# Performance work log

Hardware: AMD Instinct MI355X
Metric: run time of the kernel (lower is better)

The kernel has to match this reference:

```python
import jax, jax.numpy as jnp
import numpy as np

HIDDEN = 1024
N_HEADS = 16
HEAD_DIM = HIDDEN // N_HEADS
WINDOW = 256
HALF_W = WINDOW // 2  # 128
GLOBAL_TOKENS = (0,)


def setup_inputs() -> dict:
    key = jax.random.key(0)
    ks = jax.random.split(key, 5)
    B, S = 1, 4096
    scale = 0.02
    return {
        "x": jax.random.normal(ks[0], (B, S, HIDDEN), dtype=jnp.float32),
        "Wq": jax.random.normal(ks[1], (HIDDEN, HIDDEN), dtype=jnp.float32) * scale,
        "Wk": jax.random.normal(ks[2], (HIDDEN, HIDDEN), dtype=jnp.float32) * scale,
        "Wv": jax.random.normal(ks[3], (HIDDEN, HIDDEN), dtype=jnp.float32) * scale,
        "Wo": jax.random.normal(ks[4], (HIDDEN, HIDDEN), dtype=jnp.float32) * scale,
    }


def _longformer_mask(seq_len: int) -> jnp.ndarray:
    # sliding window |i-j| <= half_w, plus full rows/cols for global tokens
    idx = jnp.arange(seq_len)
    mask = jnp.abs(idx[:, None] - idx[None, :]) <= HALF_W
    for g in GLOBAL_TOKENS:
        if 0 <= g < seq_len:
            mask = mask.at[g, :].set(True)
            mask = mask.at[:, g].set(True)
    return mask  # [S, S] bool


def reference(x, Wq, Wk, Wv, Wo):
    B, S, H = x.shape
    scale = HEAD_DIM ** -0.5
    # nn.Linear(bias=False): y = x @ W.T ; split heads -> [B, nH, S, hd]
    def proj(W):
        return jnp.einsum('bsh,oh->bso', x, W).reshape(B, S, N_HEADS, HEAD_DIM).transpose(0, 2, 1, 3)
    q, k, v = proj(Wq), proj(Wk), proj(Wv)
    scores = jnp.einsum('bnsd,bntd->bnst', q, k) * scale  # [B, nH, S, S]
    mask = _longformer_mask(S)
    scores = jnp.where(mask[None, None], scores, jnp.float32(-jnp.inf))
    attn = jax.nn.softmax(scores, axis=-1)
    out = jnp.einsum('bnst,bntd->bnsd', attn, v)  # [B, nH, S, hd]
    out = out.transpose(0, 2, 1, 3).reshape(B, S, H)
    return jnp.einsum('bsh,oh->bso', out, Wo)
```

## Files before the change

### kernel.cpp

```cpp
#include <hip/hip_runtime.h>
#include <hip/hip_bf16.h>
#include <stdint.h>

#define S_LEN 4096
#define HID   1024
#define NH    16
#define HD    64
#define HWIN  128

typedef __bf16 bf16x8 __attribute__((ext_vector_type(8)));
typedef float  f32x4  __attribute__((ext_vector_type(4)));
typedef unsigned short u16x8 __attribute__((ext_vector_type(8)));

typedef const __attribute__((address_space(1))) unsigned int* gas_ptr;
typedef __attribute__((address_space(3))) unsigned int* las_ptr;

__device__ __forceinline__ float bf2f(unsigned short u) {
  union { float f; uint32_t i; } w; w.i = ((uint32_t)u) << 16; return w.f;
}
__device__ __forceinline__ unsigned short f2bf(float f) {
  union { float f; uint32_t i; } w; w.f = f;
  uint32_t r = (w.i + 0x7FFFu + ((w.i >> 16) & 1u)) >> 16;
  return (unsigned short)r;
}

__device__ __forceinline__ void gld_lds16(const void* g, void* l) {
  __builtin_amdgcn_global_load_lds((gas_ptr)g, (las_ptr)l, 16, 0, 0);
}

__global__ __launch_bounds__(256) void convert_all(
    const float* __restrict__ x,
    const float* __restrict__ wq, const float* __restrict__ wk,
    const float* __restrict__ wv, const float* __restrict__ wo,
    unsigned short* __restrict__ xb,
    unsigned short* __restrict__ wqb, unsigned short* __restrict__ wkb,
    unsigned short* __restrict__ wvb, unsigned short* __restrict__ wob) {
  const float* in; unsigned short* out; int n4;
  switch (blockIdx.y) {
    case 0:  in = x;  out = xb;  n4 = (S_LEN * HID) / 4; break;
    case 1:  in = wq; out = wqb; n4 = (HID * HID) / 4;   break;
    case 2:  in = wk; out = wkb; n4 = (HID * HID) / 4;   break;
    case 3:  in = wv; out = wvb; n4 = (HID * HID) / 4;   break;
    default: in = wo; out = wob; n4 = (HID * HID) / 4;   break;
  }
  int i = blockIdx.x * 256 + threadIdx.x;
  if (i >= n4) return;
  float4 v = reinterpret_cast<const float4*>(in)[i];
  ushort4 o;
  o.x = f2bf(v.x); o.y = f2bf(v.y); o.z = f2bf(v.z); o.w = f2bf(v.w);
  reinterpret_cast<ushort4*>(out)[i] = o;
}

__device__ __forceinline__ void gemm_body(const unsigned short* __restrict__ A,
                                          const unsigned short* __restrict__ B,
                                          unsigned short* __restrict__ Cb,
                                          float* __restrict__ Cf, int mode) {
  __shared__ __align__(16) unsigned short As[128 * 64];
  __shared__ __align__(16) unsigned short Bs[128 * 64];
  constexpr int K = HID;
  const int tid  = threadIdx.x;
  const int lane = tid & 63;
  const int wave = tid >> 6;
  const int wm = wave >> 1, wn = wave & 1;
  const int m0 = blockIdx.x * 128;
  const int n0 = blockIdx.y * 128;
  const int cl = lane & 15, g = lane >> 4;

  f32x4 acc[4][4];
#pragma unroll
  for (int i = 0; i < 4; i++)
#pragma unroll
    for (int j = 0; j < 4; j++) acc[i][j] = f32x4{0.f, 0.f, 0.f, 0.f};

  const unsigned short* Ap[4];
  const unsigned short* Bp[4];
  int ldso[4];
#pragma unroll
  for (int u = 0; u < 4; u++) {
    int s = tid + u * 256;
    int row = s >> 3, c16 = s & 7;
    int sc = ((c16 ^ (row & 7)) << 3);
    Ap[u] = A + (size_t)(m0 + row) * K + sc;
    Bp[u] = B + (size_t)(n0 + row) * K + sc;
    ldso[u] = s * 8;
  }

  for (int k0 = 0; k0 < K; k0 += 64) {
#pragma unroll
    for (int u = 0; u < 4; u++) {
      gld_lds16(Ap[u] + k0, &As[ldso[u]]);
      gld_lds16(Bp[u] + k0, &Bs[ldso[u]]);
    }
    __syncthreads();
#pragma unroll
    for (int kk = 0; kk < 2; kk++) {
      bf16x8 a[4], b[4];
#pragma unroll
      for (int mi = 0; mi < 4; mi++) {
        int row = wm * 64 + mi * 16 + cl;
        int c16 = (kk * 4 + g) ^ (row & 7);
        a[mi] = *reinterpret_cast<const bf16x8*>(&As[row * 64 + c16 * 8]);
      }
#pragma unroll
      for (int ni = 0; ni < 4; ni++) {
        int row = wn * 64 + ni * 16 + cl;
        int c16 = (kk * 4 + g) ^ (row & 7);
        b[ni] = *reinterpret_cast<const bf16x8*>(&Bs[row * 64 + c16 * 8]);
      }
#pragma unroll
      for (int mi = 0; mi < 4; mi++)
#pragma unroll
        for (int ni = 0; ni < 4; ni++)
          acc[mi][ni] = __builtin_amdgcn_mfma_f32_16x16x32_bf16(a[mi], b[ni], acc[mi][ni], 0, 0, 0);
    }
    __syncthreads();
  }

  const int rl = g * 4;
#pragma unroll
  for (int mi = 0; mi < 4; mi++)
#pragma unroll
    for (int ni = 0; ni < 4; ni++)
#pragma unroll
      for (int i = 0; i < 4; i++) {
        int r = m0 + wm * 64 + mi * 16 + rl + i;
        int c = n0 + wn * 64 + ni * 16 + cl;
        float v = acc[mi][ni][i];
        if (mode == 2)      Cf[(size_t)r * HID + c] = v;
        else if (mode == 1) Cb[(size_t)c * S_LEN + r] = f2bf(v);
        else                Cb[(size_t)r * HID + c] = f2bf(v);
      }
}

__global__ __launch_bounds__(256, 2) void gemm_qkv(
    const unsigned short* __restrict__ xb,
    const unsigned short* __restrict__ wqb, const unsigned short* __restrict__ wkb,
    const unsigned short* __restrict__ wvb,
    unsigned short* __restrict__ Qb, unsigned short* __restrict__ Kb,
    unsigned short* __restrict__ Vt) {
  const unsigned short* B = (blockIdx.z == 0) ? wqb : (blockIdx.z == 1) ? wkb : wvb;
  unsigned short* C       = (blockIdx.z == 0) ? Qb  : (blockIdx.z == 1) ? Kb  : Vt;
  int mode = (blockIdx.z == 2) ? 1 : 0;
  gemm_body(xb, B, C, nullptr, mode);
}

__global__ __launch_bounds__(256, 2) void gemm_proj(
    const unsigned short* __restrict__ Ob, const unsigned short* __restrict__ wob,
    float* __restrict__ out) {
  gemm_body(Ob, wob, nullptr, out, 2);
}

__global__ __launch_bounds__(256) void attn_win(
    const unsigned short* __restrict__ Qb,
    const unsigned short* __restrict__ Kb,
    const unsigned short* __restrict__ Vt,
    unsigned short* __restrict__ Ob,
    float* __restrict__ mw, float* __restrict__ lw, float* __restrict__ ow) {
  const int tid  = threadIdx.x;
  const int lane = tid & 63;
  const int wave = tid >> 6;

  if (blockIdx.x >= 1024) {
    const int bid = blockIdx.x - 1024;
    const int c = bid & 15, h = bid >> 4;
    const int k = c * 256 + tid;
    __shared__ float qsh[HD];
    __shared__ float ps[256];
    __shared__ float redm[4], redl[4];
    __shared__ float red2[4][HD];
    const float LOG2E = 1.44269504f;

    if (tid < HD) qsh[tid] = bf2f(Qb[h * HD + tid]);
    __syncthreads();

    const unsigned short* kr = Kb + (size_t)k * HID + h * HD;
    float acc = 0.f;
#pragma unroll
    for (int v8 = 0; v8 < 8; v8++) {
      u16x8 kv = *reinterpret_cast<const u16x8*>(kr + v8 * 8);
#pragma unroll
      for (int j = 0; j < 8; j++) acc += qsh[v8 * 8 + j] * bf2f(kv[j]);
    }
    float s = acc * 0.125f;

    float m = s;
#pragma unroll
    for (int d = 1; d < 64; d <<= 1) m = fmaxf(m, __shfl_xor(m, d, 64));
    if (lane == 0) redm[wave] = m;
    __syncthreads();
    float m_c = fmaxf(fmaxf(redm[0], redm[1]), fmaxf(redm[2], redm[3]));

    float p = exp2f((s - m_c) * LOG2E);
    ps[tid] = p;
    float l = p;
#pragma unroll
    for (int d = 1; d < 64; d <<= 1) l += __shfl_xor(l, d, 64);
    if (lane == 0) redl[wave] = l;
    __syncthreads();
    float l_c = redl[0] + redl[1] + redl[2] + redl[3];

    const int d = tid & 63, grp = tid >> 6;
    const unsigned short* vrow = Vt + (size_t)(h * HD + d) * S_LEN + c * 256 + grp * 64;
    float a2 = 0.f;
#pragma unroll
    for (int v8 = 0; v8 < 8; v8++) {
      u16x8 vv = *reinterpret_cast<const u16x8*>(vrow + v8 * 8);
#pragma unroll
      for (int j = 0; j < 8; j++) a2 += ps[grp * 64 + v8 * 8 + j] * bf2f(vv[j]);
    }
    red2[grp][d] = a2;
    __syncthreads();
    if (tid < HD) {
      float o = red2[0][tid] + red2[1][tid] + red2[2][tid] + red2[3][tid];
      ow[(size_t)(h * 16 + c) * HD + tid] = o;
    }
    if (tid == 0) { mw[h * 16 + c] = m_c; lw[h * 16 + c] = l_c; }
    return;
  }

  __shared__ __align__(16) unsigned short Kl[2][64 * 64];
  __shared__ __align__(16) unsigned short Vl[2][64 * 64];
  __shared__ __align__(16) unsigned short Ps[4][16 * 64];
  const int L  = (blockIdx.x & 7) * 128 + (blockIdx.x >> 3);
  const int h  = L >> 6;
  const int q0 = (L & 63) * 64;
  const int qr   = q0 + wave * 16;
  const int cl = lane & 15, g = lane >> 4, rl = g * 4;
  const float SCL = 0.125f * 1.44269504f;

  int kw0 = q0 - 128; if (kw0 < 0) kw0 = 0;
  int kw1 = q0 + 192; if (kw1 > S_LEN) kw1 = S_LEN;
  const int nc = (kw1 - kw0) >> 6;

  const int s0 = tid, s1 = tid + 256;
  const int kr0 = s0 >> 3, kc0 = ((s0 & 7) ^ (kr0 & 7)) << 3;
  const int kr1 = s1 >> 3, kc1 = ((s1 & 7) ^ (kr1 & 7)) << 3;
  const unsigned short* Kbase = Kb + h * HD;
  const unsigned short* Vbase = Vt + (size_t)h * HD * S_LEN;

  auto stage = [&](int kb, int b) {
    gld_lds16(Kbase + (size_t)(kb + kr0) * HID + kc0, &Kl[b][s0 * 8]);
    gld_lds16(Kbase + (size_t)(kb + kr1) * HID + kc1, &Kl[b][s1 * 8]);
    gld_lds16(Vbase + (size_t)kr0 * S_LEN + kb + kc0, &Vl[b][s0 * 8]);
    gld_lds16(Vbase + (size_t)kr1 * S_LEN + kb + kc1, &Vl[b][s1 * 8]);
  };

  stage(kw0, 0);

  bf16x8 qf[2], k0f[2];
  {
    const unsigned short* qb = Qb + (size_t)(qr + cl) * HID + h * HD + g * 8;
    qf[0] = *reinterpret_cast<const bf16x8*>(qb);
    qf[1] = *reinterpret_cast<const bf16x8*>(qb + 32);
    const unsigned short* k0 = Kb + h * HD + g * 8;
    k0f[0] = *reinterpret_cast<const bf16x8*>(k0);
    k0f[1] = *reinterpret_cast<const bf16x8*>(k0 + 32);
  }
  float v0[4];
#pragma unroll
  for (int nt = 0; nt < 4; nt++)
    v0[nt] = bf2f(Vt[(size_t)(h * HD + nt * 16 + cl) * S_LEN]);

  float m_i[4] = {-1e30f, -1e30f, -1e30f, -1e30f};
  float l_i[4] = {0.f, 0.f, 0.f, 0.f};
  f32x4 oacc[4];
#pragma unroll
  for (int nt = 0; nt < 4; nt++) oacc[nt] = f32x4{0.f, 0.f, 0.f, 0.f};

  __syncthreads();

  for (int c = 0; c < nc; c++) {
    const int cur = c & 1;
    const int kb = kw0 + c * 64;
    if (c + 1 < nc) stage(kw0 + (c + 1) * 64, cur ^ 1);

    bf16x8 kf[4][2];
#pragma unroll
    for (int t = 0; t < 4; t++) {
      int R = t * 16 + cl;
      kf[t][0] = *reinterpret_cast<const bf16x8*>(&Kl[cur][R * 64 + ((g ^ (R & 7)) << 3)]);
      kf[t][1] = *reinterpret_cast<const bf16x8*>(&Kl[cur][R * 64 + (((g + 4) ^ (R & 7)) << 3)]);
    }
    f32x4 s4[4];
    __builtin_amdgcn_s_setprio(1);
#pragma unroll
    for (int t = 0; t < 4; t++) {
      s4[t] = f32x4{0.f, 0.f, 0.f, 0.f};
      s4[t] = __builtin_amdgcn_mfma_f32_16x16x32_bf16(qf[0], kf[t][0], s4[t], 0, 0, 0);
      s4[t] = __builtin_amdgcn_mfma_f32_16x16x32_bf16(qf[1], kf[t][1], s4[t], 0, 0, 0);
    }
    __builtin_amdgcn_s_setprio(0);

    float sv[4][4], tm[4];
    if (kb >= qr - 113 && kb <= qr + 65) {
#pragma unroll
      for (int i = 0; i < 4; i++) {
        tm[i] = -1e30f;
#pragma unroll
        for (int t = 0; t < 4; t++) {
          float v = s4[t][i] * SCL;
          sv[t][i] = v;
          tm[i] = fmaxf(tm[i], v);
        }
      }
    } else {
#pragma unroll
      for (int i = 0; i < 4; i++) {
        int row = qr + rl + i;
        tm[i] = -1e30f;
#pragma unroll
        for (int t = 0; t < 4; t++) {
          int col = kb + t * 16 + cl;
          int d = row - col;
          float v = (d <= HWIN && d >= -HWIN) ? s4[t][i] * SCL : -1e30f;
          sv[t][i] = v;
          tm[i] = fmaxf(tm[i], v);
        }
      }
    }
#pragma unroll
    for (int dd = 1; dd < 16; dd <<= 1)
#pragma unroll
      for (int i = 0; i < 4; i++) tm[i] = fmaxf(tm[i], __shfl_xor(tm[i], dd, 16));

    float p[4][4], ps[4];
#pragma unroll
    for (int i = 0; i < 4; i++) {
      float mnew = fmaxf(m_i[i], tm[i]);
      float fac  = exp2f(m_i[i] - mnew);
      m_i[i] = mnew;
      float sum = 0.f;
#pragma unroll
      for (int t = 0; t < 4; t++) { p[t][i] = exp2f(sv[t][i] - mnew); sum += p[t][i]; }
      ps[i] = sum;
      l_i[i] *= fac;
#pragma unroll
      for (int nt = 0; nt < 4; nt++) oacc[nt][i] *= fac;
    }
#pragma unroll
    for (int dd = 1; dd < 16; dd <<= 1)
#pragma unroll
      for (int i = 0; i < 4; i++) ps[i] += __shfl_xor(ps[i], dd, 16);
#pragma unroll
    for (int i = 0; i < 4; i++) l_i[i] += ps[i];

#pragma unroll
    for (int t = 0; t < 4; t++)
#pragma unroll
      for (int i = 0; i < 4; i++) {
        int row = rl + i;
        Ps[wave][row * 64 + ((t * 16 + cl) ^ ((row & 7) << 3))] = f2bf(p[t][i]);
      }
    bf16x8 pf[2];
    pf[0] = *reinterpret_cast<const bf16x8*>(&Ps[wave][cl * 64 + ((g * 8) ^ ((cl & 7) << 3))]);
    pf[1] = *reinterpret_cast<const bf16x8*>(&Ps[wave][cl * 64 + ((32 + g * 8) ^ ((cl & 7) << 3))]);

    __builtin_amdgcn_s_setprio(1);
#pragma unroll
    for (int nt = 0; nt < 4; nt++) {
      int row = nt * 16 + cl;
      bf16x8 vf0 = *reinterpret_cast<const bf16x8*>(&Vl[cur][row * 64 + ((g ^ (row & 7)) << 3)]);
      bf16x8 vf1 = *reinterpret_cast<const bf16x8*>(&Vl[cur][row * 64 + (((g + 4) ^ (row & 7)) << 3)]);
      oacc[nt] = __builtin_amdgcn_mfma_f32_16x16x32_bf16(pf[0], vf0, oacc[nt], 0, 0, 0);
      oacc[nt] = __builtin_amdgcn_mfma_f32_16x16x32_bf16(pf[1], vf1, oacc[nt], 0, 0, 0);
    }
    __builtin_amdgcn_s_setprio(0);

    __syncthreads();
  }

  float part = 0.f;
#pragma unroll
  for (int s = 0; s < 2; s++)
#pragma unroll
    for (int j = 0; j < 8; j++) part += (float)qf[s][j] * (float)k0f[s][j];
  part += __shfl_xor(part, 16);
  part += __shfl_xor(part, 32);
  float s0q = part * SCL;
#pragma unroll
  for (int i = 0; i < 4; i++) {
    float z0 = __shfl(s0q, rl + i, 16);
    int row = qr + rl + i;
    if (row > HWIN) {
      float mnew = fmaxf(m_i[i], z0);
      float fac  = exp2f(m_i[i] - mnew);
      float p0   = exp2f(z0 - mnew);
      l_i[i] = l_i[i] * fac + p0;
#pragma unroll
      for (int nt = 0; nt < 4; nt++)
        oacc[nt][i] = oacc[nt][i] * fac + p0 * v0[nt];
    }
  }

#pragma unroll
  for (int nt = 0; nt < 4; nt++)
#pragma unroll
    for (int i = 0; i < 4; i++)
      Ob[(size_t)(qr + rl + i) * HID + h * HD + nt * 16 + cl] = f2bf(oacc[nt][i] / l_i[i]);
}

__global__ __launch_bounds__(64) void attn_row0_fin(
    const float* __restrict__ mw, const float* __restrict__ lw,
    const float* __restrict__ ow, unsigned short* __restrict__ Ob) {
  const int h = blockIdx.x, d = threadIdx.x;
  const float LOG2E = 1.44269504f;
  float m_g = -1e30f;
#pragma unroll
  for (int c = 0; c < 16; c++) m_g = fmaxf(m_g, mw[h * 16 + c]);
  float lsum = 0.f, osum = 0.f;
#pragma unroll
  for (int c = 0; c < 16; c++) {
    float w = exp2f((mw[h * 16 + c] - m_g) * LOG2E);
    lsum += lw[h * 16 + c] * w;
    osum += ow[(size_t)(h * 16 + c) * HD + d] * w;
  }
  Ob[h * HD + d] = f2bf(osum / lsum);
}

extern "C" void kernel_launch(void* const* d_in, const int* in_sizes, int n_in,
                              void* d_out, int out_size, void* d_ws, size_t ws_size,
                              hipStream_t stream) {
  const float* x  = (const float*)d_in[0];
  const float* wq = (const float*)d_in[1];
  const float* wk = (const float*)d_in[2];
  const float* wv = (const float*)d_in[3];
  const float* wo = (const float*)d_in[4];
  float* out = (float*)d_out;
  char* ws = (char*)d_ws;
  const size_t MB = 1024ull * 1024ull;
  unsigned short* xb  = (unsigned short*)(ws + 0 * MB);
  unsigned short* wqb = (unsigned short*)(ws + 8 * MB);
  unsigned short* wkb = (unsigned short*)(ws + 10 * MB);
  unsigned short* wvb = (unsigned short*)(ws + 12 * MB);
  unsigned short* wob = (unsigned short*)(ws + 14 * MB);
  unsigned short* Qb  = (unsigned short*)(ws + 16 * MB);
  unsigned short* Kb  = (unsigned short*)(ws + 24 * MB);
  unsigned short* Vt  = (unsigned short*)(ws + 32 * MB);
  unsigned short* Ob  = (unsigned short*)(ws + 40 * MB);
  float* mw = (float*)(ws + 48 * MB);
  float* lw = (float*)(ws + 48 * MB + 4096);
  float* ow = (float*)(ws + 48 * MB + 8192);

  dim3 blk(256);
  convert_all<<<dim3((S_LEN * HID / 4 + 255) / 256, 5), blk, 0, stream>>>(
      x, wq, wk, wv, wo, xb, wqb, wkb, wvb, wob);
  gemm_qkv<<<dim3(S_LEN / 128, HID / 128, 3), blk, 0, stream>>>(
      xb, wqb, wkb, wvb, Qb, Kb, Vt);
  attn_win<<<dim3(1280), blk, 0, stream>>>(Qb, Kb, Vt, Ob, mw, lw, ow);
  attn_row0_fin<<<dim3(NH), dim3(64), 0, stream>>>(mw, lw, ow, Ob);
  gemm_proj<<<dim3(S_LEN / 128, HID / 128), blk, 0, stream>>>(Ob, wob, out);
}
```

Baseline: 98.65 us.

## Tighten convert grid, stage V-transpose via LDS, fuse row-0 fixup into proj GEMM

The conversion kernel is relaunched as a 2048-block grid with no idle blocks. Each thread now handles four float4 elements spread across x and the four weight matrices. The V projection epilogue now writes its transpose through shared memory (XOR-swizzled), so global stores become 16-byte row-contiguous instead of scattered 2-byte writes. The separate row-0 global-token finalize kernel is removed and its work is done by the blockIdx.x==0 blocks of the output projection GEMM before they load Ob. This saves one launch, at the cost of some redundant work in those blocks and a dependency on store visibility within the block.

```diff
diff --git a/kernel.cpp b/kernel.cpp
--- a/kernel.cpp
+++ b/kernel.cpp
@@ -35,28 +35,38 @@
     unsigned short* __restrict__ xb,
     unsigned short* __restrict__ wqb, unsigned short* __restrict__ wkb,
     unsigned short* __restrict__ wvb, unsigned short* __restrict__ wob) {
-  const float* in; unsigned short* out; int n4;
-  switch (blockIdx.y) {
-    case 0:  in = x;  out = xb;  n4 = (S_LEN * HID) / 4; break;
-    case 1:  in = wq; out = wqb; n4 = (HID * HID) / 4;   break;
-    case 2:  in = wk; out = wkb; n4 = (HID * HID) / 4;   break;
-    case 3:  in = wv; out = wvb; n4 = (HID * HID) / 4;   break;
-    default: in = wo; out = wob; n4 = (HID * HID) / 4;   break;
-  }
+  const int XF4 = (S_LEN * HID) / 4;
+  const int WF4 = (HID * HID) / 4;
   int i = blockIdx.x * 256 + threadIdx.x;
-  if (i >= n4) return;
-  float4 v = reinterpret_cast<const float4*>(in)[i];
-  ushort4 o;
-  o.x = f2bf(v.x); o.y = f2bf(v.y); o.z = f2bf(v.z); o.w = f2bf(v.w);
-  reinterpret_cast<ushort4*>(out)[i] = o;
+#pragma unroll
+  for (int it = 0; it < 4; it++, i += 524288) {
+    const float* in; unsigned short* out; int off;
+    if (i < XF4) { in = x; out = xb; off = i; }
+    else {
+      int j = i - XF4;
+      int w = j >> 18;
+      off = j & (WF4 - 1);
+      switch (w) {
+        case 0:  in = wq; out = wqb; break;
+        case 1:  in = wk; out = wkb; break;
+        case 2:  in = wv; out = wvb; break;
+        default: in = wo; out = wob; break;
+      }
+    }
+    float4 v = reinterpret_cast<const float4*>(in)[off];
+    ushort4 o;
+    o.x = f2bf(v.x); o.y = f2bf(v.y); o.z = f2bf(v.z); o.w = f2bf(v.w);
+    reinterpret_cast<ushort4*>(out)[off] = o;
+  }
 }
 
 __device__ __forceinline__ void gemm_body(const unsigned short* __restrict__ A,
                                           const unsigned short* __restrict__ B,
                                           unsigned short* __restrict__ Cb,
                                           float* __restrict__ Cf, int mode) {
-  __shared__ __align__(16) unsigned short As[128 * 64];
-  __shared__ __align__(16) unsigned short Bs[128 * 64];
+  __shared__ __align__(16) unsigned short SM[2 * 128 * 64];
+  unsigned short* As = SM;
+  unsigned short* Bs = SM + 128 * 64;
   constexpr int K = HID;
   const int tid  = threadIdx.x;
   const int lane = tid & 63;
@@ -117,6 +127,32 @@
   }
 
   const int rl = g * 4;
+  if (mode == 1) {
+#pragma unroll
+    for (int mi = 0; mi < 4; mi++)
+#pragma unroll
+      for (int ni = 0; ni < 4; ni++) {
+        int c = wn * 64 + ni * 16 + cl;
+        int slot = (wm * 16 + mi * 4 + g) ^ ((c & 7) << 2);
+        uint2 u;
+        u.x = (uint32_t)f2bf(acc[mi][ni][0]) | ((uint32_t)f2bf(acc[mi][ni][1]) << 16);
+        u.y = (uint32_t)f2bf(acc[mi][ni][2]) | ((uint32_t)f2bf(acc[mi][ni][3]) << 16);
+        *reinterpret_cast<uint2*>(&SM[c * 128 + slot * 4]) = u;
+      }
+    __syncthreads();
+    const int rgrp = tid & 15;
+#pragma unroll
+    for (int p = 0; p < 8; p++) {
+      int c = p * 16 + (tid >> 4);
+      int s0 = (2 * rgrp) ^ ((c & 7) << 2);
+      int s1 = (2 * rgrp + 1) ^ ((c & 7) << 2);
+      uint2 a2 = *reinterpret_cast<const uint2*>(&SM[c * 128 + s0 * 4]);
+      uint2 b2 = *reinterpret_cast<const uint2*>(&SM[c * 128 + s1 * 4]);
+      uint4 o{a2.x, a2.y, b2.x, b2.y};
+      *reinterpret_cast<uint4*>(&Cb[(size_t)(n0 + c) * S_LEN + m0 + rgrp * 8]) = o;
+    }
+    return;
+  }
 #pragma unroll
   for (int mi = 0; mi < 4; mi++)
 #pragma unroll
@@ -126,9 +162,8 @@
         int r = m0 + wm * 64 + mi * 16 + rl + i;
         int c = n0 + wn * 64 + ni * 16 + cl;
         float v = acc[mi][ni][i];
-        if (mode == 2)      Cf[(size_t)r * HID + c] = v;
-        else if (mode == 1) Cb[(size_t)c * S_LEN + r] = f2bf(v);
-        else                Cb[(size_t)r * HID + c] = f2bf(v);
+        if (mode == 2) Cf[(size_t)r * HID + c] = v;
+        else           Cb[(size_t)r * HID + c] = f2bf(v);
       }
 }
 
@@ -145,8 +180,28 @@
 }
 
 __global__ __launch_bounds__(256, 2) void gemm_proj(
-    const unsigned short* __restrict__ Ob, const unsigned short* __restrict__ wob,
-    float* __restrict__ out) {
+    unsigned short* __restrict__ Ob, const unsigned short* __restrict__ wob,
+    const float* __restrict__ mw, const float* __restrict__ lw,
+    const float* __restrict__ ow, float* __restrict__ out) {
+  if (blockIdx.x == 0) {
+    const float LOG2E = 1.44269504f;
+    for (int cc = threadIdx.x; cc < HID; cc += 256) {
+      int h = cc >> 6, d = cc & 63;
+      float m_g = -1e30f;
+#pragma unroll
+      for (int c = 0; c < 16; c++) m_g = fmaxf(m_g, mw[h * 16 + c]);
+      float lsum = 0.f, osum = 0.f;
+#pragma unroll
+      for (int c = 0; c < 16; c++) {
+        float w = exp2f((mw[h * 16 + c] - m_g) * LOG2E);
+        lsum += lw[h * 16 + c] * w;
+        osum += ow[(size_t)(h * 16 + c) * HD + d] * w;
+      }
+      Ob[cc] = f2bf(osum / lsum);
+    }
+    asm volatile("s_waitcnt vmcnt(0)" ::: "memory");
+    __syncthreads();
+  }
   gemm_body(Ob, wob, nullptr, out, 2);
 }
 
@@ -397,24 +452,6 @@
 #pragma unroll
     for (int i = 0; i < 4; i++)
       Ob[(size_t)(qr + rl + i) * HID + h * HD + nt * 16 + cl] = f2bf(oacc[nt][i] / l_i[i]);
-}
-
-__global__ __launch_bounds__(64) void attn_row0_fin(
-    const float* __restrict__ mw, const float* __restrict__ lw,
-    const float* __restrict__ ow, unsigned short* __restrict__ Ob) {
-  const int h = blockIdx.x, d = threadIdx.x;
-  const float LOG2E = 1.44269504f;
-  float m_g = -1e30f;
-#pragma unroll
-  for (int c = 0; c < 16; c++) m_g = fmaxf(m_g, mw[h * 16 + c]);
-  float lsum = 0.f, osum = 0.f;
-#pragma unroll
-  for (int c = 0; c < 16; c++) {
-    float w = exp2f((mw[h * 16 + c] - m_g) * LOG2E);
-    lsum += lw[h * 16 + c] * w;
-    osum += ow[(size_t)(h * 16 + c) * HD + d] * w;
-  }
-  Ob[h * HD + d] = f2bf(osum / lsum);
 }
 
 extern "C" void kernel_launch(void* const* d_in, const int* in_sizes, int n_in,
@@ -442,11 +479,11 @@
   float* ow = (float*)(ws + 48 * MB + 8192);
 
   dim3 blk(256);
-  convert_all<<<dim3((S_LEN * HID / 4 + 255) / 256, 5), blk, 0, stream>>>(
+  convert_all<<<dim3(2048), blk, 0, stream>>>(
       x, wq, wk, wv, wo, xb, wqb, wkb, wvb, wob);
   gemm_qkv<<<dim3(S_LEN / 128, HID / 128, 3), blk, 0, stream>>>(
       xb, wqb, wkb, wvb, Qb, Kb, Vt);
   attn_win<<<dim3(1280), blk, 0, stream>>>(Qb, Kb, Vt, Ob, mw, lw, ow);
-  attn_row0_fin<<<dim3(NH), dim3(64), 0, stream>>>(mw, lw, ow, Ob);
-  gemm_proj<<<dim3(S_LEN / 128, HID / 128), blk, 0, stream>>>(Ob, wob, out);
-}
+  gemm_proj<<<dim3(S_LEN / 128, HID / 128), blk, 0, stream>>>(
+      Ob, wob, mw, lw, ow, out);
+}
```

Result: faster. 91.53 us (-7.2%).
